# Kernel optimization log

Measured on AMD Instinct MI355X. Metric: run time of the kernel, lower is better.

The kernel has to match this reference:

```python
import jax, jax.numpy as jnp
import numpy as np

EPS = 1e-5

def _ln(x, g, b):
    # layer norm over last dim
    m = jnp.mean(x, axis=-1, keepdims=True)
    v = jnp.mean((x - m) ** 2, axis=-1, keepdims=True)
    return (x - m) * jax.lax.rsqrt(v + EPS) * g + b

def setup_inputs() -> dict:
    key = jax.random.key(0)
    ks = jax.random.split(key, 12)
    B, T, E, H, OUT = 128, 256, 64, 128, 1
    GENOME = 1_000_000
    D = 2 * E  # input_size_lstm
    inp = {}
    inp["indices"] = jax.random.randint(ks[0], (B, T, 2), 0, GENOME, dtype=jnp.int64)
    inp["h0"] = jax.random.normal(ks[1], (B, H), dtype=jnp.float32)
    inp["c0"] = jax.random.normal(ks[2], (B, H), dtype=jnp.float32)
    inp["embed_table"] = jax.random.normal(ks[3], (GENOME, E), dtype=jnp.float32)
    s_ih = 1.0 / np.sqrt(D)
    s_hh = 1.0 / np.sqrt(H)
    inp["W_ih"] = jax.random.uniform(ks[4], (4 * H, D), minval=-s_ih, maxval=s_ih, dtype=jnp.float32)
    inp["W_hh"] = jax.random.uniform(ks[5], (4 * H, H), minval=-s_hh, maxval=s_hh, dtype=jnp.float32)
    inp["g_ih"] = jnp.ones((4 * H,), jnp.float32)
    inp["b_ih"] = jnp.zeros((4 * H,), jnp.float32)
    inp["g_hh"] = jnp.ones((4 * H,), jnp.float32)
    inp["b_hh"] = jnp.zeros((4 * H,), jnp.float32)
    inp["g_c"] = jnp.ones((H,), jnp.float32)
    inp["b_c"] = jnp.zeros((H,), jnp.float32)
    s_o = 1.0 / np.sqrt(H * T)
    inp["W_out"] = jax.random.uniform(ks[6], (OUT * T, H * T), minval=-s_o, maxval=s_o, dtype=jnp.float32)
    inp["b_out"] = jax.random.uniform(ks[7], (OUT * T,), minval=-s_o, maxval=s_o, dtype=jnp.float32)
    return inp

def _forward(indices, embed_table, W_ih, W_hh, g_ih, b_ih, g_hh, b_hh, g_c, b_c, W_out, b_out, h0, c0):
    B, T = indices.shape[0], indices.shape[1]
    H = h0.shape[-1]
    # embedding gather: (B,T,2,E) -> (B,T,2E)
    emb = embed_table[indices].reshape(B, T, -1)
    # precompute input-to-hidden gates for all timesteps: (B,T,4H)
    x_gates = jnp.einsum("btd,gd->btg", emb, W_ih)

    def step(carry, xg):
        h, c = carry
        gates = _ln(xg, g_ih, b_ih) + _ln(h @ W_hh.T, g_hh, b_hh)
        i, f, g, o = jnp.split(gates, 4, axis=-1)
        c_new = jax.nn.sigmoid(f) * c + jax.nn.sigmoid(i) * jnp.tanh(g)
        h_new = jax.nn.sigmoid(o) * jnp.tanh(_ln(c_new, g_c, b_c))
        return (h_new, c_new), h_new

    (_, _), hs = jax.lax.scan(step, (h0, c0), jnp.swapaxes(x_gates, 0, 1))
    # hs: (T,B,H) -> (B,T*H)
    seq_out = jnp.swapaxes(hs, 0, 1).reshape(B, T * H)
    out = jax.nn.sigmoid(seq_out @ W_out.T + b_out)
    return out, emb

def reference(indices, h0, c0, embed_table, W_ih, W_hh, g_ih, b_ih, g_hh, b_hh, g_c, b_c, W_out, b_out):
    return _forward(indices, embed_table, W_ih, W_hh, g_ih, b_ih, g_hh, b_hh, g_c, b_c, W_out, b_out, h0, c0)
```

## Files before the change

kernel.cpp:

```cpp
#include <hip/hip_runtime.h>
#include <cstddef>


__device__ __forceinline__ float sigm(float x) { return 1.0f / (1.0f + __expf(-x)); }

__global__ void k_embed(const int* __restrict__ idx, const float4* __restrict__ table4,
                        float4* __restrict__ emb4) {
  int i = blockIdx.x * blockDim.x + threadIdx.x;
  int p = i >> 4, j = i & 15;
  int id = idx[p];
  emb4[(size_t)p * 16 + j] = table4[(size_t)id * 16 + j];
}

__global__ void k_transpose(const float* __restrict__ W, float* __restrict__ Wt) {
  int i = blockIdx.x * 256 + threadIdx.x;
  int g = i >> 7, k = i & 127;
  Wt[k * 512 + g] = W[i];
}

__global__ __launch_bounds__(256) void k_gemm_tn(
    const float* __restrict__ A, const float* __restrict__ Bm, float* __restrict__ C,
    int K, int kchunks, int N, size_t partstride)
{
  __shared__ float As[64][65];
  __shared__ float Bs[64][68];
  const int tid = threadIdx.x;
  const int tx = tid & 15, ty = tid >> 4;
  const int m0 = blockIdx.x * 64, n0 = blockIdx.y * 64;
  float acc[4][4] = {};
  size_t kbase = (size_t)blockIdx.z * kchunks * 64;
  for (int kc = 0; kc < kchunks; ++kc) {
    size_t k0 = kbase + (size_t)kc * 64;
    #pragma unroll
    for (int it = 0; it < 4; ++it) {
      int fi = it * 256 + tid;
      int row = fi >> 4, col4 = fi & 15;
      float4 va = *(const float4*)(A + (size_t)(m0 + row) * K + k0 + col4 * 4);
      As[row][col4*4+0] = va.x; As[row][col4*4+1] = va.y;
      As[row][col4*4+2] = va.z; As[row][col4*4+3] = va.w;
      float4 vb = *(const float4*)(Bm + (size_t)(n0 + row) * K + k0 + col4 * 4);
      Bs[col4*4+0][row] = vb.x; Bs[col4*4+1][row] = vb.y;
      Bs[col4*4+2][row] = vb.z; Bs[col4*4+3][row] = vb.w;
    }
    __syncthreads();
    #pragma unroll 8
    for (int k = 0; k < 64; ++k) {
      float a0 = As[ty*4+0][k], a1 = As[ty*4+1][k], a2 = As[ty*4+2][k], a3 = As[ty*4+3][k];
      float b0 = Bs[k][tx*4+0], b1 = Bs[k][tx*4+1], b2 = Bs[k][tx*4+2], b3 = Bs[k][tx*4+3];
      acc[0][0] += a0*b0; acc[0][1] += a0*b1; acc[0][2] += a0*b2; acc[0][3] += a0*b3;
      acc[1][0] += a1*b0; acc[1][1] += a1*b1; acc[1][2] += a1*b2; acc[1][3] += a1*b3;
      acc[2][0] += a2*b0; acc[2][1] += a2*b1; acc[2][2] += a2*b2; acc[2][3] += a2*b3;
      acc[3][0] += a3*b0; acc[3][1] += a3*b1; acc[3][2] += a3*b2; acc[3][3] += a3*b3;
    }
    __syncthreads();
  }
  float* Cp = C + (size_t)blockIdx.z * partstride;
  #pragma unroll
  for (int i = 0; i < 4; ++i) {
    float4 v = make_float4(acc[i][0], acc[i][1], acc[i][2], acc[i][3]);
    *(float4*)(Cp + (size_t)(m0 + ty*4 + i) * N + n0 + tx*4) = v;
  }
}

__global__ __launch_bounds__(512) void k_scan(
    const float* __restrict__ xg,
    const float* __restrict__ Wt,
    const float* __restrict__ h0, const float* __restrict__ c0,
    const float* __restrict__ g_ih, const float* __restrict__ b_ih,
    const float* __restrict__ g_hh, const float* __restrict__ b_hh,
    const float* __restrict__ g_c,  const float* __restrict__ b_c,
    float* __restrict__ hs)
{
  const int b = blockIdx.x;
  const int g = threadIdx.x;
  const int lane = g & 63, wave = g >> 6;

  __shared__ float h_s[128];
  __shared__ float gates_s[512];
  __shared__ float red[8][4];
  __shared__ float red2[2][2];

  float w[128];
  #pragma unroll
  for (int k = 0; k < 128; ++k) w[k] = Wt[k * 512 + g];

  const float gihv = g_ih[g], bihv = b_ih[g];
  const float ghhv = g_hh[g], bhhv = b_hh[g];
  float gcv = 0.f, bcv = 0.f, cval = 0.f;
  if (g < 128) {
    gcv = g_c[g]; bcv = b_c[g];
    cval = c0[b * 128 + g];
    h_s[g] = h0[b * 128 + g];
  }
  __syncthreads();

  const float* xgb = xg + (size_t)b * 256 * 512;
  float* hsb = hs + (size_t)b * 256 * 128;
  const float inv512 = 1.0f / 512.0f, inv128 = 1.0f / 128.0f;

  for (int t = 0; t < 256; ++t) {
    float xv = xgb[t * 512 + g];
    float acc = 0.f;
    #pragma unroll
    for (int k = 0; k < 128; ++k) acc += w[k] * h_s[k];

    float s0 = xv, s1 = xv * xv, s2 = acc, s3 = acc * acc;
    #pragma unroll
    for (int off = 32; off; off >>= 1) {
      s0 += __shfl_xor(s0, off);
      s1 += __shfl_xor(s1, off);
      s2 += __shfl_xor(s2, off);
      s3 += __shfl_xor(s3, off);
    }
    if (lane == 0) { red[wave][0] = s0; red[wave][1] = s1; red[wave][2] = s2; red[wave][3] = s3; }
    __syncthreads();
    float t0 = 0, t1 = 0, t2 = 0, t3 = 0;
    #pragma unroll
    for (int i2 = 0; i2 < 8; ++i2) { t0 += red[i2][0]; t1 += red[i2][1]; t2 += red[i2][2]; t3 += red[i2][3]; }
    float mx = t0 * inv512, vx = t1 * inv512 - mx * mx;
    float mh = t2 * inv512, vh = t3 * inv512 - mh * mh;
    float lnx = (xv - mx) * rsqrtf(vx + 1e-5f) * gihv + bihv;
    float lnh = (acc - mh) * rsqrtf(vh + 1e-5f) * ghhv + bhhv;
    gates_s[g] = lnx + lnh;
    __syncthreads();

    float cn = 0.f, ov = 0.f;
    if (g < 128) {
      float iv = gates_s[g], fv = gates_s[128 + g], gv = gates_s[256 + g];
      ov = gates_s[384 + g];
      cn = sigm(fv) * cval + sigm(iv) * tanhf(gv);
      cval = cn;
    }
    float u0 = cn, u1 = cn * cn;
    #pragma unroll
    for (int off = 32; off; off >>= 1) { u0 += __shfl_xor(u0, off); u1 += __shfl_xor(u1, off); }
    if (g < 128 && lane == 0) { red2[wave][0] = u0; red2[wave][1] = u1; }
    __syncthreads();
    if (g < 128) {
      float sm = red2[0][0] + red2[1][0], sq = red2[0][1] + red2[1][1];
      float mc = sm * inv128, vc = sq * inv128 - mc * mc;
      float lnc = (cn - mc) * rsqrtf(vc + 1e-5f) * gcv + bcv;
      float hn = sigm(ov) * tanhf(lnc);
      h_s[g] = hn;
      hsb[t * 128 + g] = hn;
    }
    __syncthreads();
  }
}

__global__ void k_reduce(const float* __restrict__ part, const float* __restrict__ b_out,
                         float* __restrict__ out) {
  int i = blockIdx.x * 256 + threadIdx.x;
  float s = b_out[i & 255];
  #pragma unroll
  for (int z = 0; z < 32; ++z) s += part[(size_t)z * 32768 + i];
  out[i] = sigm(s);
}

extern "C" void kernel_launch(void* const* d_in, const int* in_sizes, int n_in,
                              void* d_out, int out_size, void* d_ws, size_t ws_size,
                              hipStream_t stream) {
  const int*   idx   = (const int*)  d_in[0];
  const float* h0    = (const float*)d_in[1];
  const float* c0    = (const float*)d_in[2];
  const float* table = (const float*)d_in[3];
  const float* W_ih  = (const float*)d_in[4];
  const float* W_hh  = (const float*)d_in[5];
  const float* g_ih  = (const float*)d_in[6];
  const float* b_ih  = (const float*)d_in[7];
  const float* g_hh  = (const float*)d_in[8];
  const float* b_hh  = (const float*)d_in[9];
  const float* g_c   = (const float*)d_in[10];
  const float* b_c   = (const float*)d_in[11];
  const float* W_out = (const float*)d_in[12];
  const float* b_out = (const float*)d_in[13];

  float* out  = (float*)d_out;
  float* emb  = out + 32768;
  float* ws   = (float*)d_ws;
  float* xg   = ws;
  float* hsb  = ws + 16777216;
  float* wt   = ws + 20971520;
  float* part = ws + 21037056;

  k_embed<<<4096, 256, 0, stream>>>(idx, (const float4*)table, (float4*)emb);
  k_transpose<<<256, 256, 0, stream>>>(W_hh, wt);
  k_gemm_tn<<<dim3(512, 8, 1), 256, 0, stream>>>(emb, W_ih, xg, 128, 2, 512, 0);
  k_scan<<<128, 512, 0, stream>>>(xg, wt, h0, c0, g_ih, b_ih, g_hh, b_hh, g_c, b_c, hsb);
  k_gemm_tn<<<dim3(2, 4, 32), 256, 0, stream>>>(hsb, W_out, part, 32768, 16, 256, 32768);
  k_reduce<<<128, 256, 0, stream>>>(part, b_out, out);
}
```

Measured before the change: 698.9 us.

## Cut LSTM scan barriers by computing the cell update redundantly in every wave

Each of the 8 waves now keeps its own copy of h in LDS and recomputes all 128 cell and hidden values itself. This removes two of the three block-wide barriers per timestep and uses double-buffered shared arrays for the gate pre-activations. The input layer-norm statistics are moved into a separate k_xstats kernel that runs before the scan, so the serial loop only reduces the recurrent gate stats. Sigmoid and tanh now use a hardware reciprocal and an exp-based tanh. The cost is extra redundant per-wave work and LDS traffic, plus slightly less accurate transcendentals.

```diff
diff --git a/kernel.cpp b/kernel.cpp
--- a/kernel.cpp
+++ b/kernel.cpp
@@ -2,7 +2,12 @@
 #include <cstddef>
 
 
-__device__ __forceinline__ float sigm(float x) { return 1.0f / (1.0f + __expf(-x)); }
+__device__ __forceinline__ float frcp(float x) { return __builtin_amdgcn_rcpf(x); }
+__device__ __forceinline__ float sigm(float x) { return frcp(1.0f + __expf(-x)); }
+__device__ __forceinline__ float ftanh(float x) {
+  float e = __expf(2.0f * x);
+  return (e - 1.0f) * frcp(e + 1.0f);
+}
 
 __global__ void k_embed(const int* __restrict__ idx, const float4* __restrict__ table4,
                         float4* __restrict__ emb4) {
@@ -62,9 +67,27 @@
   }
 }
 
-__global__ __launch_bounds__(512) void k_scan(
+__global__ __launch_bounds__(256) void k_xstats(const float4* __restrict__ xg4,
+                                                float* __restrict__ xm, float* __restrict__ xr) {
+  int row = blockIdx.x * 4 + (threadIdx.x >> 6);
+  int lane = threadIdx.x & 63;
+  const float4* r = xg4 + (size_t)row * 128;
+  float4 a = r[lane], b = r[lane + 64];
+  float s = a.x + a.y + a.z + a.w + b.x + b.y + b.z + b.w;
+  float q = a.x*a.x + a.y*a.y + a.z*a.z + a.w*a.w + b.x*b.x + b.y*b.y + b.z*b.z + b.w*b.w;
+  #pragma unroll
+  for (int off = 32; off; off >>= 1) { s += __shfl_xor(s, off); q += __shfl_xor(q, off); }
+  if (lane == 0) {
+    float m = s * (1.0f / 512.0f);
+    xm[row] = m;
+    xr[row] = rsqrtf(q * (1.0f / 512.0f) - m * m + 1e-5f);
+  }
+}
+
+__global__ __launch_bounds__(512, 2) void k_scan(
     const float* __restrict__ xg,
     const float* __restrict__ Wt,
+    const float* __restrict__ xm, const float* __restrict__ xr,
     const float* __restrict__ h0, const float* __restrict__ c0,
     const float* __restrict__ g_ih, const float* __restrict__ b_ih,
     const float* __restrict__ g_hh, const float* __restrict__ b_hh,
@@ -75,76 +98,93 @@
   const int g = threadIdx.x;
   const int lane = g & 63, wave = g >> 6;
 
-  __shared__ float h_s[128];
-  __shared__ float gates_s[512];
-  __shared__ float red[8][4];
-  __shared__ float red2[2][2];
-
-  float w[128];
-  #pragma unroll
-  for (int k = 0; k < 128; ++k) w[k] = Wt[k * 512 + g];
-
-  const float gihv = g_ih[g], bihv = b_ih[g];
-  const float ghhv = g_hh[g], bhhv = b_hh[g];
-  float gcv = 0.f, bcv = 0.f, cval = 0.f;
-  if (g < 128) {
-    gcv = g_c[g]; bcv = b_c[g];
-    cval = c0[b * 128 + g];
-    h_s[g] = h0[b * 128 + g];
-  }
-  __syncthreads();
+  __shared__ float xv_s[2][512];
+  __shared__ float acc_s[2][512];
+  __shared__ float2 red_s[2][8];
+  __shared__ float4 h4_s[8][32];
+
+  float4 w4[32];
+  #pragma unroll
+  for (int k = 0; k < 32; ++k) {
+    w4[k].x = Wt[(4*k+0) * 512 + g];
+    w4[k].y = Wt[(4*k+1) * 512 + g];
+    w4[k].z = Wt[(4*k+2) * 512 + g];
+    w4[k].w = Wt[(4*k+3) * 512 + g];
+  }
+  #pragma unroll
+  for (int k = 0; k < 32; ++k)
+    asm volatile("" : "+v"(w4[k].x), "+v"(w4[k].y), "+v"(w4[k].z), "+v"(w4[k].w));
+
+  float gih[8], bih[8], ghh[8], bhh[8];
+  #pragma unroll
+  for (int j = 0; j < 8; ++j) {
+    gih[j] = g_ih[j*64 + lane]; bih[j] = b_ih[j*64 + lane];
+    ghh[j] = g_hh[j*64 + lane]; bhh[j] = b_hh[j*64 + lane];
+  }
+  float gc0 = g_c[lane], bc0 = b_c[lane], gc1 = g_c[64 + lane], bc1 = b_c[64 + lane];
+  float cv0 = c0[b*128 + lane], cv1 = c0[b*128 + 64 + lane];
+
+  float* hown = (float*)&h4_s[wave][0];
+  hown[lane]      = h0[b*128 + lane];
+  hown[64 + lane] = h0[b*128 + 64 + lane];
 
   const float* xgb = xg + (size_t)b * 256 * 512;
+  const float* xmb = xm + b * 256;
+  const float* xrb = xr + b * 256;
   float* hsb = hs + (size_t)b * 256 * 128;
-  const float inv512 = 1.0f / 512.0f, inv128 = 1.0f / 128.0f;
 
   for (int t = 0; t < 256; ++t) {
-    float xv = xgb[t * 512 + g];
-    float acc = 0.f;
-    #pragma unroll
-    for (int k = 0; k < 128; ++k) acc += w[k] * h_s[k];
-
-    float s0 = xv, s1 = xv * xv, s2 = acc, s3 = acc * acc;
-    #pragma unroll
-    for (int off = 32; off; off >>= 1) {
-      s0 += __shfl_xor(s0, off);
-      s1 += __shfl_xor(s1, off);
-      s2 += __shfl_xor(s2, off);
-      s3 += __shfl_xor(s3, off);
-    }
-    if (lane == 0) { red[wave][0] = s0; red[wave][1] = s1; red[wave][2] = s2; red[wave][3] = s3; }
+    const int buf = t & 1;
+    float xv = xgb[t*512 + g];
+    xv_s[buf][g] = xv;
+    float mx = xmb[t], rx = xrb[t];
+
+    float a0 = 0.f, a1 = 0.f, a2 = 0.f, a3 = 0.f;
+    #pragma unroll
+    for (int k = 0; k < 32; ++k) {
+      float4 h4 = h4_s[wave][k];
+      a0 += w4[k].x * h4.x; a1 += w4[k].y * h4.y;
+      a2 += w4[k].z * h4.z; a3 += w4[k].w * h4.w;
+    }
+    float acc = (a0 + a1) + (a2 + a3);
+    acc_s[buf][g] = acc;
+
+    float s = acc, q = acc * acc;
+    #pragma unroll
+    for (int off = 32; off; off >>= 1) { s += __shfl_xor(s, off); q += __shfl_xor(q, off); }
+    if (lane == 0) red_s[buf][wave] = make_float2(s, q);
+
     __syncthreads();
-    float t0 = 0, t1 = 0, t2 = 0, t3 = 0;
-    #pragma unroll
-    for (int i2 = 0; i2 < 8; ++i2) { t0 += red[i2][0]; t1 += red[i2][1]; t2 += red[i2][2]; t3 += red[i2][3]; }
-    float mx = t0 * inv512, vx = t1 * inv512 - mx * mx;
-    float mh = t2 * inv512, vh = t3 * inv512 - mh * mh;
-    float lnx = (xv - mx) * rsqrtf(vx + 1e-5f) * gihv + bihv;
-    float lnh = (acc - mh) * rsqrtf(vh + 1e-5f) * ghhv + bhhv;
-    gates_s[g] = lnx + lnh;
-    __syncthreads();
-
-    float cn = 0.f, ov = 0.f;
-    if (g < 128) {
-      float iv = gates_s[g], fv = gates_s[128 + g], gv = gates_s[256 + g];
-      ov = gates_s[384 + g];
-      cn = sigm(fv) * cval + sigm(iv) * tanhf(gv);
-      cval = cn;
-    }
-    float u0 = cn, u1 = cn * cn;
-    #pragma unroll
-    for (int off = 32; off; off >>= 1) { u0 += __shfl_xor(u0, off); u1 += __shfl_xor(u1, off); }
-    if (g < 128 && lane == 0) { red2[wave][0] = u0; red2[wave][1] = u1; }
-    __syncthreads();
-    if (g < 128) {
-      float sm = red2[0][0] + red2[1][0], sq = red2[0][1] + red2[1][1];
-      float mc = sm * inv128, vc = sq * inv128 - mc * mc;
-      float lnc = (cn - mc) * rsqrtf(vc + 1e-5f) * gcv + bcv;
-      float hn = sigm(ov) * tanhf(lnc);
-      h_s[g] = hn;
-      hsb[t * 128 + g] = hn;
-    }
-    __syncthreads();
+
+    float rsx = 0.f, rsq = 0.f;
+    #pragma unroll
+    for (int i = 0; i < 8; ++i) { float2 v = red_s[buf][i]; rsx += v.x; rsq += v.y; }
+    float mh = rsx * (1.0f/512.0f), vh = rsq * (1.0f/512.0f) - mh * mh;
+    float rh = rsqrtf(vh + 1e-5f);
+
+    float gv[8];
+    #pragma unroll
+    for (int j = 0; j < 8; ++j) {
+      int p = j*64 + lane;
+      float lx = (xv_s[buf][p]  - mx) * rx * gih[j] + bih[j];
+      float lh = (acc_s[buf][p] - mh) * rh * ghh[j] + bhh[j];
+      gv[j] = lx + lh;
+    }
+    float cn0 = sigm(gv[2]) * cv0 + sigm(gv[0]) * ftanh(gv[4]);
+    float cn1 = sigm(gv[3]) * cv1 + sigm(gv[1]) * ftanh(gv[5]);
+    cv0 = cn0; cv1 = cn1;
+
+    float cs = cn0 + cn1, cq = cn0*cn0 + cn1*cn1;
+    #pragma unroll
+    for (int off = 32; off; off >>= 1) { cs += __shfl_xor(cs, off); cq += __shfl_xor(cq, off); }
+    float mc = cs * (1.0f/128.0f), vc = cq * (1.0f/128.0f) - mc * mc;
+    float rc = rsqrtf(vc + 1e-5f);
+
+    float hn0 = sigm(gv[6]) * ftanh((cn0 - mc) * rc * gc0 + bc0);
+    float hn1 = sigm(gv[7]) * ftanh((cn1 - mc) * rc * gc1 + bc1);
+    hown[lane]      = hn0;
+    hown[64 + lane] = hn1;
+    if (wave == 0) { hsb[t*128 + lane] = hn0; hsb[t*128 + 64 + lane] = hn1; }
   }
 }
 
@@ -182,11 +222,14 @@
   float* hsb  = ws + 16777216;
   float* wt   = ws + 20971520;
   float* part = ws + 21037056;
+  float* xmv  = part;
+  float* xrv  = part + 32768;
 
   k_embed<<<4096, 256, 0, stream>>>(idx, (const float4*)table, (float4*)emb);
   k_transpose<<<256, 256, 0, stream>>>(W_hh, wt);
   k_gemm_tn<<<dim3(512, 8, 1), 256, 0, stream>>>(emb, W_ih, xg, 128, 2, 512, 0);
-  k_scan<<<128, 512, 0, stream>>>(xg, wt, h0, c0, g_ih, b_ih, g_hh, b_hh, g_c, b_c, hsb);
+  k_xstats<<<8192, 256, 0, stream>>>((const float4*)xg, xmv, xrv);
+  k_scan<<<128, 512, 0, stream>>>(xg, wt, xmv, xrv, h0, c0, g_ih, b_ih, g_hh, b_hh, g_c, b_c, hsb);
   k_gemm_tn<<<dim3(2, 4, 32), 256, 0, stream>>>(hsb, W_out, part, 32768, 16, 256, 32768);
   k_reduce<<<128, 256, 0, stream>>>(part, b_out, out);
 }
```

Result: faster. 611.9 us (-12.4%).
